# Performance work log

Measured on AMD Instinct MI355X. Metric: run time of the kernel, lower is better.

## Reference

```python
import jax, jax.numpy as jnp
import numpy as np

H = 256      # SPELLER_HIDDEN_SIZE
CTX = 128    # CONTEXT_SIZE
V = 33       # num_chars
L = 3        # SPELLER_LAYERS


def setup_inputs() -> dict:
    key = jax.random.key(0)
    ks = jax.random.split(key, 14)
    B, T = 1024, 220
    s = 0.05
    f = lambda k, shape: (jax.random.normal(k, shape, dtype=jnp.float32) * s)
    return {
        "labels": jax.random.randint(ks[0], (B, T), 0, V),
        "embed": f(ks[1], (V, H)),
        "Wih0": f(ks[2], (4 * H, H + CTX)),          # layer 0 input-hidden
        "Wih_rest": f(ks[3], (L - 1, 4 * H, H)),      # layers 1..2
        "Whh": f(ks[4], (L, 4 * H, H)),
        "bih": f(ks[5], (L, 4 * H)),
        "bhh": f(ks[6], (L, 4 * H)),
        "W1": f(ks[7], (H, H + CTX)),
        "b1": f(ks[8], (H,)),
        "W2": f(ks[9], (V, H)),
        "b2": f(ks[10], (V,)),
        "h0": f(ks[11], (L, H)),
        "c0": f(ks[12], (L, H)),
    }


def _lstm_cell(x, h, c, Wi, Wh, bi, bh):
    # torch LSTMCell: gates in (i, f, g, o) order
    g = x @ Wi.T + bi + h @ Wh.T + bh
    i, f, gg, o = jnp.split(g, 4, axis=-1)
    c2 = jax.nn.sigmoid(f) * c + jax.nn.sigmoid(i) * jnp.tanh(gg)
    h2 = jax.nn.sigmoid(o) * jnp.tanh(c2)
    return h2, c2


def reference(labels, embed, Wih0, Wih_rest, Whh, bih, bhh, W1, b1, W2, b2, h0, c0):
    B, T = labels.shape
    ctx = jnp.zeros((B, CTX), dtype=embed.dtype)  # context never updated in this module
    Wis = [Wih0, Wih_rest[0], Wih_rest[1]]

    def step(carry, _):
        char, h, c = carry          # h, c: [L, B, H]
        x = jnp.concatenate([embed[char], ctx], axis=1)   # [B, H+CTX]
        hs, cs = [], []
        for l in range(L):
            hn, cn = _lstm_cell(x, h[l], c[l], Wis[l], Whh[l], bih[l], bhh[l])
            hs.append(hn); cs.append(cn)
            x = hn
        feat = jnp.concatenate([x, ctx], axis=1)           # [B, H+CTX]
        pred = jnp.maximum(feat @ W1.T + b1, 0.0) @ W2.T + b2  # [B, V]
        char = jnp.argmax(pred, axis=1)                    # greedy decoding (eval mode)
        return (char, jnp.stack(hs), jnp.stack(cs)), pred

    char0 = jnp.zeros((B,), dtype=jnp.int32)
    h_init = jnp.broadcast_to(h0[:, None, :], (L, B, H))
    c_init = jnp.broadcast_to(c0[:, None, :], (L, B, H))
    _, preds = jax.lax.scan(step, (char0, h_init, c_init), None, length=T)
    return preds.transpose(1, 0, 2)  # [B, T, V] (torch stacks along dim=1)
```

## Files before the change

### kernel.cpp

```cpp
#include <hip/hip_runtime.h>
#include <math.h>

#define NW     64
#define NT     256
#define H      256
#define CTX    128
#define V      33
#define T      220
#define BATCH  1024
#define SENT   0xAAAAAAAAu

#define WS_H0  64
#define WS_H1  (WS_H0 + T*H)
#define WS_H2  (WS_H1 + T*H)
#define WS_F   (WS_H2 + T*H)
#define WS_PR  (WS_F  + T*H)

__device__ __forceinline__ float gld(const float* p) {
  return __hip_atomic_load(p, __ATOMIC_RELAXED, __HIP_MEMORY_SCOPE_AGENT);
}
__device__ __forceinline__ void gst(float* p, float v) {
  __hip_atomic_store(p, v, __ATOMIC_RELAXED, __HIP_MEMORY_SCOPE_AGENT);
}
__device__ __forceinline__ float sigf(float x) { return 1.f / (1.f + expf(-x)); }

__device__ __forceinline__ float red16(float a) {
  #pragma unroll
  for (int m = 8; m; m >>= 1) a += __shfl_xor(a, m, 16);
  return a;
}

__device__ __forceinline__ float dot16r(const float4* __restrict__ w,
                                        const float* __restrict__ xsh, int lane) {
  const float4* x4 = reinterpret_cast<const float4*>(xsh) + lane * 4;
  float a = 0.f;
  #pragma unroll
  for (int m = 0; m < 4; ++m) {
    float4 W = w[m], X = x4[m];
    a += W.x * X.x + W.y * X.y + W.z * X.z + W.w * X.w;
  }
  return a;
}

__device__ __forceinline__ float pollw(const float* p) {
  float v = gld(p);
  while (__float_as_uint(v) == SENT) v = gld(p);
  return v;
}

__global__ __launch_bounds__(NT) void speller_persistent(
    const float* __restrict__ embed,
    const float* __restrict__ Wih0,
    const float* __restrict__ Wih_rest,
    const float* __restrict__ Whh,
    const float* __restrict__ bih,
    const float* __restrict__ bhh,
    const float* __restrict__ W1,
    const float* __restrict__ b1,
    const float* __restrict__ W2,
    const float* __restrict__ b2,
    const float* __restrict__ h0,
    const float* __restrict__ c0,
    float* __restrict__ ws)
{
  __shared__ __align__(16) float sh_w[V * H];
  __shared__ __align__(16) float sh_h0p[H];
  __shared__ __align__(16) float sh_h1p[H];
  __shared__ __align__(16) float sh_h2p[H];
  __shared__ __align__(16) float sh_fv[H];
  __shared__ float sh_emb_tab[V * 16];
  __shared__ float sh_b2[V];
  __shared__ float sh_g[16];
  __shared__ float sh_logits[V];
  __shared__ int   sh_char;

  const int tid  = threadIdx.x, wg = blockIdx.x;
  const int r    = tid >> 4, lane = tid & 15;
  const int gate = r >> 2,  jj   = r & 3;
  const int wrow = gate * H + wg * 4 + jj;

  unsigned* cnt = reinterpret_cast<unsigned*>(ws);
  float* HX0 = ws + WS_H0;
  float* HX1 = ws + WS_H1;
  float* HX2 = ws + WS_H2;
  float* FX  = ws + WS_F;
  float* PR  = ws + WS_PR;

  float4 w_hh0[4], w_ih1[4], w_hh1[4], w_ih2[4], w_hh2[4], w1r[4];
  {
    const float4* p;
    p = reinterpret_cast<const float4*>(Whh + (size_t)wrow * H) + lane * 4;
    w_hh0[0]=p[0]; w_hh0[1]=p[1]; w_hh0[2]=p[2]; w_hh0[3]=p[3];
    p = reinterpret_cast<const float4*>(Wih_rest + (size_t)wrow * H) + lane * 4;
    w_ih1[0]=p[0]; w_ih1[1]=p[1]; w_ih1[2]=p[2]; w_ih1[3]=p[3];
    p = reinterpret_cast<const float4*>(Whh + (size_t)(1024 + wrow) * H) + lane * 4;
    w_hh1[0]=p[0]; w_hh1[1]=p[1]; w_hh1[2]=p[2]; w_hh1[3]=p[3];
    p = reinterpret_cast<const float4*>(Wih_rest + (size_t)(1024 + wrow) * H) + lane * 4;
    w_ih2[0]=p[0]; w_ih2[1]=p[1]; w_ih2[2]=p[2]; w_ih2[3]=p[3];
    p = reinterpret_cast<const float4*>(Whh + (size_t)(2048 + wrow) * H) + lane * 4;
    w_hh2[0]=p[0]; w_hh2[1]=p[1]; w_hh2[2]=p[2]; w_hh2[3]=p[3];
  }
  const float bsum1 = bih[1024 + wrow] + bhh[1024 + wrow];
  const float bsum2 = bih[2048 + wrow] + bhh[2048 + wrow];

  float b1r = 0.f;
  w1r[0] = w1r[1] = w1r[2] = w1r[3] = float4{0.f, 0.f, 0.f, 0.f};
  if (tid < 64) {
    const int jf = wg * 4 + (tid >> 4);
    b1r = b1[jf];
    const float4* p = reinterpret_cast<const float4*>(W1 + (size_t)jf * (H + CTX)) + lane * 4;
    w1r[0]=p[0]; w1r[1]=p[1]; w1r[2]=p[2]; w1r[3]=p[3];
  }

  float c0r = 0.f, c1r = 0.f, c2r = 0.f;
  if (tid < 4) {
    c0r = c0[0 * H + wg * 4 + tid];
    c1r = c0[1 * H + wg * 4 + tid];
    c2r = c0[2 * H + wg * 4 + tid];
  }
  sh_h0p[tid] = h0[0 * H + tid];
  sh_h1p[tid] = h0[1 * H + tid];
  sh_h2p[tid] = h0[2 * H + tid];
  if (tid < V) sh_b2[tid] = b2[tid];

  for (int i = tid; i < V * H; i += NT) sh_w[i] = embed[i];
  __syncthreads();
  {
    const float4* w4 = reinterpret_cast<const float4*>(
        Wih0 + (size_t)wrow * (H + CTX) + lane * 16);
    const float4 q0 = w4[0], q1 = w4[1], q2 = w4[2], q3 = w4[3];
    const float bs = bih[wrow] + bhh[wrow];
    for (int v = 0; v < V; ++v) {
      const float4* e4 = reinterpret_cast<const float4*>(sh_w + v * H + lane * 16);
      float4 e0 = e4[0], e1 = e4[1], e2 = e4[2], e3 = e4[3];
      float a = q0.x*e0.x + q0.y*e0.y + q0.z*e0.z + q0.w*e0.w
              + q1.x*e1.x + q1.y*e1.y + q1.z*e1.z + q1.w*e1.w
              + q2.x*e2.x + q2.y*e2.y + q2.z*e2.z + q2.w*e2.w
              + q3.x*e3.x + q3.y*e3.y + q3.z*e3.z + q3.w*e3.w;
      a = red16(a);
      if (lane == 0) sh_emb_tab[v * 16 + r] = a + bs;
    }
  }
  __syncthreads();
  for (int i = tid; i < V * H; i += NT) sh_w[i] = W2[i];

  if (tid < T) {
    const int t = tid;
    const float sf = __uint_as_float(SENT);
    #pragma unroll
    for (int k = 0; k < 4; ++k) {
      gst(HX0 + t * H + wg * 4 + k, sf);
      gst(HX1 + t * H + wg * 4 + k, sf);
      gst(HX2 + t * H + wg * 4 + k, sf);
      gst(FX  + t * H + wg * 4 + k, sf);
    }
  }

  __syncthreads();
  if (tid == 0) {
    __hip_atomic_fetch_add(cnt, 1u, __ATOMIC_RELEASE, __HIP_MEMORY_SCOPE_AGENT);
    while (__hip_atomic_load(cnt, __ATOMIC_ACQUIRE, __HIP_MEMORY_SCOPE_AGENT)
           < (unsigned)NW)
      __builtin_amdgcn_s_sleep(1);
  }
  __syncthreads();

  for (int t = 0; t < T; ++t) {
    float acc = dot16r(w_hh0, sh_h0p, lane);
    acc = red16(acc);
    int chr = 0;
    if (t > 0) {
      sh_fv[tid] = pollw(FX + (size_t)(t - 1) * H + tid);
      __syncthreads();
      const int v = tid >> 2, s = tid & 3;
      if (v < V) {
        const float4* wv = reinterpret_cast<const float4*>(sh_w + v * H) + s * 16;
        const float4* fq = reinterpret_cast<const float4*>(sh_fv) + s * 16;
        float a = 0.f;
        #pragma unroll
        for (int m = 0; m < 16; ++m) {
          float4 Wq = wv[m], Fq = fq[m];
          a += Wq.x*Fq.x + Wq.y*Fq.y + Wq.z*Fq.z + Wq.w*Fq.w;
        }
        a += __shfl_xor(a, 1, 4);
        a += __shfl_xor(a, 2, 4);
        if (s == 0) sh_logits[v] = a + sh_b2[v];
      }
      __syncthreads();
      if (tid == 0) {
        float best = sh_logits[0]; int bv = 0;
        for (int v2 = 1; v2 < V; ++v2)
          if (sh_logits[v2] > best) { best = sh_logits[v2]; bv = v2; }
        sh_char = bv;
      }
      __syncthreads();
      chr = sh_char;
      if (wg == 0 && tid < V) PR[(t - 1) * V + tid] = sh_logits[tid];
    }
    if (lane == 0) sh_g[r] = acc + sh_emb_tab[chr * 16 + r];
    __syncthreads();
    if (tid < 4) {
      float gi = sh_g[tid], gf = sh_g[4 + tid], gg = sh_g[8 + tid], go = sh_g[12 + tid];
      float cn = sigf(gf) * c0r + sigf(gi) * tanhf(gg);
      c0r = cn;
      gst(HX0 + (size_t)t * H + wg * 4 + tid, sigf(go) * tanhf(cn));
    }

    {
      float hv = pollw(HX0 + (size_t)t * H + tid);
      sh_h0p[tid] = hv;
    }
    __syncthreads();
    acc = dot16r(w_ih1, sh_h0p, lane) + dot16r(w_hh1, sh_h1p, lane);
    acc = red16(acc);
    if (lane == 0) sh_g[r] = acc + bsum1;
    __syncthreads();
    if (tid < 4) {
      float gi = sh_g[tid], gf = sh_g[4 + tid], gg = sh_g[8 + tid], go = sh_g[12 + tid];
      float cn = sigf(gf) * c1r + sigf(gi) * tanhf(gg);
      c1r = cn;
      gst(HX1 + (size_t)t * H + wg * 4 + tid, sigf(go) * tanhf(cn));
    }

    {
      float hv = pollw(HX1 + (size_t)t * H + tid);
      sh_h1p[tid] = hv;
    }
    __syncthreads();
    acc = dot16r(w_ih2, sh_h1p, lane) + dot16r(w_hh2, sh_h2p, lane);
    acc = red16(acc);
    if (lane == 0) sh_g[r] = acc + bsum2;
    __syncthreads();
    if (tid < 4) {
      float gi = sh_g[tid], gf = sh_g[4 + tid], gg = sh_g[8 + tid], go = sh_g[12 + tid];
      float cn = sigf(gf) * c2r + sigf(gi) * tanhf(gg);
      c2r = cn;
      gst(HX2 + (size_t)t * H + wg * 4 + tid, sigf(go) * tanhf(cn));
    }

    {
      float hv = pollw(HX2 + (size_t)t * H + tid);
      sh_h2p[tid] = hv;
    }
    __syncthreads();
    if (tid < 64) {
      float a = dot16r(w1r, sh_h2p, lane);
      a = red16(a);
      if (lane == 0)
        gst(FX + (size_t)t * H + wg * 4 + (tid >> 4), fmaxf(a + b1r, 0.f));
    }
  }

  if (wg == 0) {
    sh_fv[tid] = pollw(FX + (size_t)(T - 1) * H + tid);
    __syncthreads();
    const int v = tid >> 2, s = tid & 3;
    if (v < V) {
      const float4* wv = reinterpret_cast<const float4*>(sh_w + v * H) + s * 16;
      const float4* fq = reinterpret_cast<const float4*>(sh_fv) + s * 16;
      float a = 0.f;
      #pragma unroll
      for (int m = 0; m < 16; ++m) {
        float4 Wq = wv[m], Fq = fq[m];
        a += Wq.x*Fq.x + Wq.y*Fq.y + Wq.z*Fq.z + Wq.w*Fq.w;
      }
      a += __shfl_xor(a, 1, 4);
      a += __shfl_xor(a, 2, 4);
      if (s == 0) sh_logits[v] = a + sh_b2[v];
    }
    __syncthreads();
    if (tid < V) PR[(T - 1) * V + tid] = sh_logits[tid];
  }
}

__global__ __launch_bounds__(NT) void bcast_kernel(const float* __restrict__ PR,
                                                   float* __restrict__ out) {
  float* o = out + (size_t)blockIdx.x * (T * V);
  for (int i = threadIdx.x; i < T * V; i += NT) o[i] = PR[i];
}

extern "C" void kernel_launch(void* const* d_in, const int* in_sizes, int n_in,
                              void* d_out, int out_size, void* d_ws, size_t ws_size,
                              hipStream_t stream) {
  const float* embed    = (const float*)d_in[1];
  const float* Wih0     = (const float*)d_in[2];
  const float* Wih_rest = (const float*)d_in[3];
  const float* Whh      = (const float*)d_in[4];
  const float* bih      = (const float*)d_in[5];
  const float* bhh      = (const float*)d_in[6];
  const float* W1       = (const float*)d_in[7];
  const float* b1       = (const float*)d_in[8];
  const float* W2       = (const float*)d_in[9];
  const float* b2       = (const float*)d_in[10];
  const float* h0       = (const float*)d_in[11];
  const float* c0       = (const float*)d_in[12];
  float* out = (float*)d_out;
  float* ws  = (float*)d_ws;

  hipMemsetAsync(d_ws, 0, 256, stream);

  speller_persistent<<<NW, NT, 0, stream>>>(embed, Wih0, Wih_rest, Whh, bih, bhh,
                                            W1, b1, W2, b2, h0, c0, ws);
  bcast_kernel<<<BATCH, NT, 0, stream>>>(ws + WS_PR, out);
}
```

Before: 2.382 ms.

## Replicate classifier MLP per block to drop FX grid exchange and reorder gates per wavefront

New measurement: 3.470 ms. +45.7%, slower.

```diff
diff --git a/kernel.cpp b/kernel.cpp
--- a/kernel.cpp
+++ b/kernel.cpp
@@ -13,8 +13,7 @@
 #define WS_H0  64
 #define WS_H1  (WS_H0 + T*H)
 #define WS_H2  (WS_H1 + T*H)
-#define WS_F   (WS_H2 + T*H)
-#define WS_PR  (WS_F  + T*H)
+#define WS_PR  (WS_H2 + T*H)
 
 __device__ __forceinline__ float gld(const float* p) {
   return __hip_atomic_load(p, __ATOMIC_RELAXED, __HIP_MEMORY_SCOPE_AGENT);
@@ -30,9 +29,9 @@
   return a;
 }
 
-__device__ __forceinline__ float dot16r(const float4* __restrict__ w,
-                                        const float* __restrict__ xsh, int lane) {
-  const float4* x4 = reinterpret_cast<const float4*>(xsh) + lane * 4;
+__device__ __forceinline__ float dot16s(const float4* __restrict__ w,
+                                        const float* __restrict__ xsh, int lane16) {
+  const float4* x4 = reinterpret_cast<const float4*>(xsh) + lane16 * 4;
   float a = 0.f;
   #pragma unroll
   for (int m = 0; m < 4; ++m) {
@@ -48,7 +47,7 @@
   return v;
 }
 
-__global__ __launch_bounds__(NT) void speller_persistent(
+__global__ __launch_bounds__(NT, 1) void speller_persistent(
     const float* __restrict__ embed,
     const float* __restrict__ Wih0,
     const float* __restrict__ Wih_rest,
@@ -67,92 +66,88 @@
   __shared__ __align__(16) float sh_h0p[H];
   __shared__ __align__(16) float sh_h1p[H];
   __shared__ __align__(16) float sh_h2p[H];
-  __shared__ __align__(16) float sh_fv[H];
-  __shared__ float sh_emb_tab[V * 16];
-  __shared__ float sh_b2[V];
-  __shared__ float sh_g[16];
+  __shared__ __align__(16) float sh_f[H];
+  __shared__ float sh_tab[V * 16];
+  __shared__ float sh_b1[H];
+  __shared__ float sh_b2v[V];
   __shared__ float sh_logits[V];
   __shared__ int   sh_char;
 
-  const int tid  = threadIdx.x, wg = blockIdx.x;
-  const int r    = tid >> 4, lane = tid & 15;
-  const int gate = r >> 2,  jj   = r & 3;
-  const int wrow = gate * H + wg * 4 + jj;
+  const int tid = threadIdx.x, wg = blockIdx.x;
+  const int jj = tid >> 6, l = tid & 63, gate = l >> 4, lane16 = l & 15;
+  const int hidx = wg * 4 + jj;
+  const int wrow = gate * H + hidx;
+  const int rr = tid >> 4, ll = tid & 15;
 
   unsigned* cnt = reinterpret_cast<unsigned*>(ws);
   float* HX0 = ws + WS_H0;
   float* HX1 = ws + WS_H1;
   float* HX2 = ws + WS_H2;
-  float* FX  = ws + WS_F;
   float* PR  = ws + WS_PR;
 
-  float4 w_hh0[4], w_ih1[4], w_hh1[4], w_ih2[4], w_hh2[4], w1r[4];
+  float4 w_hh0[4], w_ih1[4], w_hh1[4], w_ih2[4], w_hh2[4];
   {
     const float4* p;
-    p = reinterpret_cast<const float4*>(Whh + (size_t)wrow * H) + lane * 4;
+    p = reinterpret_cast<const float4*>(Whh + (size_t)wrow * H) + lane16 * 4;
     w_hh0[0]=p[0]; w_hh0[1]=p[1]; w_hh0[2]=p[2]; w_hh0[3]=p[3];
-    p = reinterpret_cast<const float4*>(Wih_rest + (size_t)wrow * H) + lane * 4;
+    p = reinterpret_cast<const float4*>(Wih_rest + (size_t)wrow * H) + lane16 * 4;
     w_ih1[0]=p[0]; w_ih1[1]=p[1]; w_ih1[2]=p[2]; w_ih1[3]=p[3];
-    p = reinterpret_cast<const float4*>(Whh + (size_t)(1024 + wrow) * H) + lane * 4;
+    p = reinterpret_cast<const float4*>(Whh + (size_t)(1024 + wrow) * H) + lane16 * 4;
     w_hh1[0]=p[0]; w_hh1[1]=p[1]; w_hh1[2]=p[2]; w_hh1[3]=p[3];
-    p = reinterpret_cast<const float4*>(Wih_rest + (size_t)(1024 + wrow) * H) + lane * 4;
+    p = reinterpret_cast<const float4*>(Wih_rest + (size_t)(1024 + wrow) * H) + lane16 * 4;
     w_ih2[0]=p[0]; w_ih2[1]=p[1]; w_ih2[2]=p[2]; w_ih2[3]=p[3];
-    p = reinterpret_cast<const float4*>(Whh + (size_t)(2048 + wrow) * H) + lane * 4;
+    p = reinterpret_cast<const float4*>(Whh + (size_t)(2048 + wrow) * H) + lane16 * 4;
     w_hh2[0]=p[0]; w_hh2[1]=p[1]; w_hh2[2]=p[2]; w_hh2[3]=p[3];
   }
   const float bsum1 = bih[1024 + wrow] + bhh[1024 + wrow];
   const float bsum2 = bih[2048 + wrow] + bhh[2048 + wrow];
 
-  float b1r = 0.f;
-  w1r[0] = w1r[1] = w1r[2] = w1r[3] = float4{0.f, 0.f, 0.f, 0.f};
-  if (tid < 64) {
-    const int jf = wg * 4 + (tid >> 4);
-    b1r = b1[jf];
-    const float4* p = reinterpret_cast<const float4*>(W1 + (size_t)jf * (H + CTX)) + lane * 4;
-    w1r[0]=p[0]; w1r[1]=p[1]; w1r[2]=p[2]; w1r[3]=p[3];
-  }
-
-  float c0r = 0.f, c1r = 0.f, c2r = 0.f;
-  if (tid < 4) {
-    c0r = c0[0 * H + wg * 4 + tid];
-    c1r = c0[1 * H + wg * 4 + tid];
-    c2r = c0[2 * H + wg * 4 + tid];
-  }
+  float4 w1c[16][4];
+  #pragma unroll
+  for (int p = 0; p < 16; ++p) {
+    const float4* q = reinterpret_cast<const float4*>(
+        W1 + (size_t)(p * 16 + rr) * (H + CTX)) + ll * 4;
+    w1c[p][0]=q[0]; w1c[p][1]=q[1]; w1c[p][2]=q[2]; w1c[p][3]=q[3];
+  }
+
+  float c0r = c0[0 * H + hidx];
+  float c1r = c0[1 * H + hidx];
+  float c2r = c0[2 * H + hidx];
+
   sh_h0p[tid] = h0[0 * H + tid];
   sh_h1p[tid] = h0[1 * H + tid];
   sh_h2p[tid] = h0[2 * H + tid];
-  if (tid < V) sh_b2[tid] = b2[tid];
+  sh_b1[tid]  = b1[tid];
+  if (tid < V) sh_b2v[tid] = b2[tid];
 
   for (int i = tid; i < V * H; i += NT) sh_w[i] = embed[i];
   __syncthreads();
   {
     const float4* w4 = reinterpret_cast<const float4*>(
-        Wih0 + (size_t)wrow * (H + CTX) + lane * 16);
+        Wih0 + (size_t)wrow * (H + CTX) + lane16 * 16);
     const float4 q0 = w4[0], q1 = w4[1], q2 = w4[2], q3 = w4[3];
     const float bs = bih[wrow] + bhh[wrow];
     for (int v = 0; v < V; ++v) {
-      const float4* e4 = reinterpret_cast<const float4*>(sh_w + v * H + lane * 16);
+      const float4* e4 = reinterpret_cast<const float4*>(sh_w + v * H + lane16 * 16);
       float4 e0 = e4[0], e1 = e4[1], e2 = e4[2], e3 = e4[3];
       float a = q0.x*e0.x + q0.y*e0.y + q0.z*e0.z + q0.w*e0.w
               + q1.x*e1.x + q1.y*e1.y + q1.z*e1.z + q1.w*e1.w
               + q2.x*e2.x + q2.y*e2.y + q2.z*e2.z + q2.w*e2.w
               + q3.x*e3.x + q3.y*e3.y + q3.z*e3.z + q3.w*e3.w;
       a = red16(a);
-      if (lane == 0) sh_emb_tab[v * 16 + r] = a + bs;
+      if (lane16 == 0) sh_tab[v * 16 + gate * 4 + jj] = a + bs;
     }
   }
   __syncthreads();
   for (int i = tid; i < V * H; i += NT) sh_w[i] = W2[i];
 
   if (tid < T) {
-    const int t = tid;
     const float sf = __uint_as_float(SENT);
     #pragma unroll
     for (int k = 0; k < 4; ++k) {
-      gst(HX0 + t * H + wg * 4 + k, sf);
-      gst(HX1 + t * H + wg * 4 + k, sf);
-      gst(HX2 + t * H + wg * 4 + k, sf);
-      gst(FX  + t * H + wg * 4 + k, sf);
+      gst(HX0 + (size_t)tid * H + wg * 4 + k, sf);
+      gst(HX1 + (size_t)tid * H + wg * 4 + k, sf);
+      gst(HX2 + (size_t)tid * H + wg * 4 + k, sf);
     }
   }
 
@@ -161,116 +156,104 @@
     __hip_atomic_fetch_add(cnt, 1u, __ATOMIC_RELEASE, __HIP_MEMORY_SCOPE_AGENT);
     while (__hip_atomic_load(cnt, __ATOMIC_ACQUIRE, __HIP_MEMORY_SCOPE_AGENT)
            < (unsigned)NW)
-      __builtin_amdgcn_s_sleep(1);
-  }
-  __syncthreads();
-
-  for (int t = 0; t < T; ++t) {
-    float acc = dot16r(w_hh0, sh_h0p, lane);
-    acc = red16(acc);
-    int chr = 0;
-    if (t > 0) {
-      sh_fv[tid] = pollw(FX + (size_t)(t - 1) * H + tid);
-      __syncthreads();
-      const int v = tid >> 2, s = tid & 3;
-      if (v < V) {
-        const float4* wv = reinterpret_cast<const float4*>(sh_w + v * H) + s * 16;
-        const float4* fq = reinterpret_cast<const float4*>(sh_fv) + s * 16;
-        float a = 0.f;
-        #pragma unroll
-        for (int m = 0; m < 16; ++m) {
-          float4 Wq = wv[m], Fq = fq[m];
-          a += Wq.x*Fq.x + Wq.y*Fq.y + Wq.z*Fq.z + Wq.w*Fq.w;
-        }
-        a += __shfl_xor(a, 1, 4);
-        a += __shfl_xor(a, 2, 4);
-        if (s == 0) sh_logits[v] = a + sh_b2[v];
-      }
-      __syncthreads();
-      if (tid == 0) {
-        float best = sh_logits[0]; int bv = 0;
-        for (int v2 = 1; v2 < V; ++v2)
-          if (sh_logits[v2] > best) { best = sh_logits[v2]; bv = v2; }
-        sh_char = bv;
-      }
-      __syncthreads();
-      chr = sh_char;
-      if (wg == 0 && tid < V) PR[(t - 1) * V + tid] = sh_logits[tid];
-    }
-    if (lane == 0) sh_g[r] = acc + sh_emb_tab[chr * 16 + r];
-    __syncthreads();
-    if (tid < 4) {
-      float gi = sh_g[tid], gf = sh_g[4 + tid], gg = sh_g[8 + tid], go = sh_g[12 + tid];
-      float cn = sigf(gf) * c0r + sigf(gi) * tanhf(gg);
-      c0r = cn;
-      gst(HX0 + (size_t)t * H + wg * 4 + tid, sigf(go) * tanhf(cn));
-    }
-
-    {
-      float hv = pollw(HX0 + (size_t)t * H + tid);
-      sh_h0p[tid] = hv;
-    }
-    __syncthreads();
-    acc = dot16r(w_ih1, sh_h0p, lane) + dot16r(w_hh1, sh_h1p, lane);
-    acc = red16(acc);
-    if (lane == 0) sh_g[r] = acc + bsum1;
-    __syncthreads();
-    if (tid < 4) {
-      float gi = sh_g[tid], gf = sh_g[4 + tid], gg = sh_g[8 + tid], go = sh_g[12 + tid];
-      float cn = sigf(gf) * c1r + sigf(gi) * tanhf(gg);
-      c1r = cn;
-      gst(HX1 + (size_t)t * H + wg * 4 + tid, sigf(go) * tanhf(cn));
-    }
-
-    {
-      float hv = pollw(HX1 + (size_t)t * H + tid);
-      sh_h1p[tid] = hv;
-    }
-    __syncthreads();
-    acc = dot16r(w_ih2, sh_h1p, lane) + dot16r(w_hh2, sh_h2p, lane);
-    acc = red16(acc);
-    if (lane == 0) sh_g[r] = acc + bsum2;
-    __syncthreads();
-    if (tid < 4) {
-      float gi = sh_g[tid], gf = sh_g[4 + tid], gg = sh_g[8 + tid], go = sh_g[12 + tid];
-      float cn = sigf(gf) * c2r + sigf(gi) * tanhf(gg);
-      c2r = cn;
-      gst(HX2 + (size_t)t * H + wg * 4 + tid, sigf(go) * tanhf(cn));
-    }
-
-    {
-      float hv = pollw(HX2 + (size_t)t * H + tid);
-      sh_h2p[tid] = hv;
-    }
-    __syncthreads();
-    if (tid < 64) {
-      float a = dot16r(w1r, sh_h2p, lane);
+      __builtin_amdgcn_s_sleep(8);
+  }
+  __syncthreads();
+
+  auto classify = [&]() {
+    const float4* x4 = reinterpret_cast<const float4*>(sh_h2p) + ll * 4;
+    const float4 X0 = x4[0], X1 = x4[1], X2 = x4[2], X3 = x4[3];
+    #pragma unroll
+    for (int p = 0; p < 16; ++p) {
+      float a = 0.f;
+      a += w1c[p][0].x*X0.x + w1c[p][0].y*X0.y + w1c[p][0].z*X0.z + w1c[p][0].w*X0.w;
+      a += w1c[p][1].x*X1.x + w1c[p][1].y*X1.y + w1c[p][1].z*X1.z + w1c[p][1].w*X1.w;
+      a += w1c[p][2].x*X2.x + w1c[p][2].y*X2.y + w1c[p][2].z*X2.z + w1c[p][2].w*X2.w;
+      a += w1c[p][3].x*X3.x + w1c[p][3].y*X3.y + w1c[p][3].z*X3.z + w1c[p][3].w*X3.w;
       a = red16(a);
-      if (lane == 0)
-        gst(FX + (size_t)t * H + wg * 4 + (tid >> 4), fmaxf(a + b1r, 0.f));
-    }
-  }
-
-  if (wg == 0) {
-    sh_fv[tid] = pollw(FX + (size_t)(T - 1) * H + tid);
+      if (ll == 0) sh_f[p * 16 + rr] = fmaxf(a + sh_b1[p * 16 + rr], 0.f);
+    }
     __syncthreads();
     const int v = tid >> 2, s = tid & 3;
     if (v < V) {
       const float4* wv = reinterpret_cast<const float4*>(sh_w + v * H) + s * 16;
-      const float4* fq = reinterpret_cast<const float4*>(sh_fv) + s * 16;
+      const float4* fv = reinterpret_cast<const float4*>(sh_f) + s * 16;
       float a = 0.f;
       #pragma unroll
       for (int m = 0; m < 16; ++m) {
-        float4 Wq = wv[m], Fq = fq[m];
+        float4 Wq = wv[m], Fq = fv[m];
         a += Wq.x*Fq.x + Wq.y*Fq.y + Wq.z*Fq.z + Wq.w*Fq.w;
       }
       a += __shfl_xor(a, 1, 4);
       a += __shfl_xor(a, 2, 4);
-      if (s == 0) sh_logits[v] = a + sh_b2[v];
-    }
-    __syncthreads();
-    if (tid < V) PR[(T - 1) * V + tid] = sh_logits[tid];
-  }
+      if (s == 0) sh_logits[v] = a + sh_b2v[v];
+    }
+    __syncthreads();
+  };
+
+  auto lstm_h = [&](float a, float& creg) -> float {
+    float gi = __shfl(a,  0, 64);
+    float gf = __shfl(a, 16, 64);
+    float gg = __shfl(a, 32, 64);
+    float go = __shfl(a, 48, 64);
+    float cn = sigf(gf) * creg + sigf(gi) * tanhf(gg);
+    creg = cn;
+    return sigf(go) * tanhf(cn);
+  };
+
+  float a0 = red16(dot16s(w_hh0, sh_h0p, lane16));
+
+  for (int t = 0; t < T; ++t) {
+    int chr = 0;
+    if (t > 0) {
+      classify();
+      if (tid < 64) {
+        float bv = (tid < V) ? sh_logits[tid] : -1e30f;
+        int   bi = tid;
+        #pragma unroll
+        for (int m = 32; m; m >>= 1) {
+          float ov = __shfl_xor(bv, m, 64);
+          int   oi = __shfl_xor(bi, m, 64);
+          if (ov > bv || (ov == bv && oi < bi)) { bv = ov; bi = oi; }
+        }
+        if (tid == 0) sh_char = bi;
+      }
+      __syncthreads();
+      chr = sh_char;
+      if (wg == 0 && tid < V) PR[(size_t)(t - 1) * V + tid] = sh_logits[tid];
+    }
+
+    {
+      float a = a0 + sh_tab[chr * 16 + gate * 4 + jj];
+      float hv = lstm_h(a, c0r);
+      if (l == 0) gst(HX0 + (size_t)t * H + hidx, hv);
+    }
+
+    float a1h = dot16s(w_hh1, sh_h1p, lane16);
+    sh_h0p[tid] = pollw(HX0 + (size_t)t * H + tid);
+    __syncthreads();
+    {
+      float a = red16(a1h + dot16s(w_ih1, sh_h0p, lane16)) + bsum1;
+      float hv = lstm_h(a, c1r);
+      if (l == 0) gst(HX1 + (size_t)t * H + hidx, hv);
+    }
+
+    float a2h = dot16s(w_hh2, sh_h2p, lane16);
+    sh_h1p[tid] = pollw(HX1 + (size_t)t * H + tid);
+    __syncthreads();
+    {
+      float a = red16(a2h + dot16s(w_ih2, sh_h1p, lane16)) + bsum2;
+      float hv = lstm_h(a, c2r);
+      if (l == 0) gst(HX2 + (size_t)t * H + hidx, hv);
+    }
+
+    a0 = red16(dot16s(w_hh0, sh_h0p, lane16));
+    sh_h2p[tid] = pollw(HX2 + (size_t)t * H + tid);
+    __syncthreads();
+  }
+
+  classify();
+  if (wg == 0 && tid < V) PR[(size_t)(T - 1) * V + tid] = sh_logits[tid];
 }
 
 __global__ __launch_bounds__(NT) void bcast_kernel(const float* __restrict__ PR,
```
